# Optimization experiments

Hardware: AMD Instinct MI355X
Metric: run time of the kernel (lower is better)

The kernel has to match this reference:

```python
import jax, jax.numpy as jnp
import numpy as np

B, S, DIM, HEADS, DH = 1, 192, 512, 8, 64
LN_EPS = 1e-5


def setup_inputs() -> dict:
    key = jax.random.key(0)
    ks = jax.random.split(key, 5)
    rn = lambda k, shp: jax.random.normal(k, shp, dtype=jnp.float32) * 0.02
    return {
        "x": jax.random.normal(ks[0], (B, S, DIM), dtype=jnp.float32),
        "ln_w": jnp.ones((DIM,), jnp.float32),
        "ln_b": jnp.zeros((DIM,), jnp.float32),
        "W_abcde": rn(ks[1], (5 * HEADS * DH, DIM)),
        "b_abcde": jnp.zeros((5 * HEADS * DH,), jnp.float32),
        "W_K": rn(ks[2], (HEADS, DH, DH, DH)),
        "W_V": rn(ks[3], (HEADS, DH, DH, DH)),
        "W_out": rn(ks[4], (DIM, HEADS * DH)),
        "b_out": jnp.zeros((DIM,), jnp.float32),
    }


def reference(x, ln_w, ln_b, W_abcde, b_abcde, W_K, W_V, W_out, b_out):
    b, n, _ = x.shape
    # LayerNorm (biased variance, eps=1e-5, affine)
    mu = jnp.mean(x, axis=-1, keepdims=True)
    var = jnp.var(x, axis=-1, keepdims=True)
    xn = (x - mu) / jnp.sqrt(var + LN_EPS) * ln_w + ln_b
    # abcde projection, chunk into 5, split heads -> [b, n, h, d]
    proj = xn @ W_abcde.T + b_abcde
    a_, b_, c_, d_, e_ = [t.reshape(b, n, HEADS, DH) for t in jnp.split(proj, 5, axis=-1)]
    # cubic attention score chain (note: heads summed out in step2, reintroduced by a_)
    step1 = jnp.einsum('brnk,nijk->brij', c_, W_K)          # [b, r, d, d]
    step2 = jnp.einsum('brij,bqnj->briq', step1, b_)        # [b, r, d, q] (sum over heads of b_)
    attn = jnp.einsum('briq,bpni->bnpqr', step2, a_)        # [b, h, p, q, r]
    # "causal" mask: positions where p >= q set to 1e-6 (faithful to masked_fill_)
    t_idx = jnp.arange(n)[:, None, None]
    s_idx = jnp.arange(n)[None, :, None]
    mask = (t_idx >= s_idx)[None, None]                      # [1,1,p,q,1]
    attn = jnp.where(mask, jnp.float32(1e-6), attn)
    # 'b n p1 p2 p3 -> b n p3 (p1 p2)', scale by 1/dim_head, softmax over (p1 p2)
    attn = attn.transpose(0, 1, 4, 2, 3).reshape(b, HEADS, n, n * n) / DH
    attn = jax.nn.softmax(attn, axis=-1)
    # pairwise values: [b, p1, p2, h, d] -> 'b p s n h -> b n h (p s)'
    v = jnp.einsum('bpnh,bqng,nhgf->bpqnf', d_, e_, W_V)
    v = v.transpose(0, 3, 4, 1, 2).reshape(b, HEADS, DH, n * n)
    # weighted sum over pair axis, merge heads
    z = jnp.einsum('bnql,bnhl->bqnh', attn, v).reshape(b, n, HEADS * DH)
    return z @ W_out.T + b_out
```

## Files before the change

### kernel.cpp

```cpp
#include <hip/hip_runtime.h>
#include <hip/hip_bf16.h>
#include <cstdint>

#define SEQ 192

typedef float f32x4 __attribute__((ext_vector_type(4)));
typedef float f32x8 __attribute__((ext_vector_type(8)));
typedef __bf16 bf16;
typedef __bf16 bf16x8 __attribute__((ext_vector_type(8)));
typedef __bf16 bf16x4 __attribute__((ext_vector_type(4)));

#define MFMA_BF16(a, b, c) __builtin_amdgcn_mfma_f32_16x16x32_bf16(a, b, c, 0, 0, 0)

__device__ __forceinline__ bf16x8 cvt8(f32x8 v) {
  bf16x8 o;
#pragma unroll
  for (int i = 0; i < 8; i++) o[i] = (bf16)v[i];
  return o;
}

__global__ __launch_bounds__(256) void k1_prep(
    const float* __restrict__ x, const float* __restrict__ ln_w, const float* __restrict__ ln_b,
    const float* __restrict__ WV, bf16* __restrict__ xn_bf, bf16* __restrict__ WVt2) {
  int bid = blockIdx.x, tid = threadIdx.x;
  if (bid < 512) {
    int g = bid & 63, hh = bid >> 6;
    __shared__ float ld[64 * 65];
    int f = tid & 63, r4 = tid >> 6;
#pragma unroll
    for (int it = 0; it < 16; it++) {
      int hp = it * 4 + r4;
      ld[hp * 65 + f] = WV[(((size_t)(hh * 64 + hp) * 64 + g) * 64) + f];
    }
    __syncthreads();
    int hp2 = tid & 63;
#pragma unroll
    for (int it = 0; it < 16; it++) {
      int ff = it * 4 + r4;
      WVt2[(size_t)hh * 262144 + (size_t)(ff * 64 + g) * 64 + hp2] = (bf16)ld[hp2 * 65 + ff];
    }
    return;
  }
  bid -= 512;
  {
    int r = bid;
    const float* xr = x + (size_t)r * 512;
    float v0 = xr[tid], v1 = xr[tid + 256];
    float s = v0 + v1, s2 = v0 * v0 + v1 * v1;
#pragma unroll
    for (int off = 32; off > 0; off >>= 1) {
      s += __shfl_down(s, off);
      s2 += __shfl_down(s2, off);
    }
    __shared__ float redS[4], redS2[4];
    int wave = tid >> 6, lane = tid & 63;
    if (lane == 0) { redS[wave] = s; redS2[wave] = s2; }
    __syncthreads();
    float S = redS[0] + redS[1] + redS[2] + redS[3];
    float S2 = redS2[0] + redS2[1] + redS2[2] + redS2[3];
    float mean = S * (1.0f / 512.0f);
    float var = S2 * (1.0f / 512.0f) - mean * mean;
    float rstd = rsqrtf(var + 1e-5f);
    bf16* xnr = xn_bf + (size_t)r * 512;
    xnr[tid] = (bf16)((v0 - mean) * rstd * ln_w[tid] + ln_b[tid]);
    xnr[tid + 256] = (bf16)((v1 - mean) * rstd * ln_w[tid + 256] + ln_b[tid + 256]);
  }
}

__device__ __forceinline__ void gemm_rm(const bf16* __restrict__ A, const bf16* __restrict__ Bt,
                                        bf16* __restrict__ C1, int N, int K, int nb, int mb,
                                        int tid) {
  int n0 = nb * 64, m0 = mb * 64;
  int wave = tid >> 6, lane = tid & 63;
  int lq = lane >> 4, l16 = lane & 15;
  const bf16* Ap = A + (size_t)(m0 + wave * 16 + l16) * K;
  f32x4 acc[4];
#pragma unroll
  for (int nt = 0; nt < 4; nt++) acc[nt] = (f32x4){0.f, 0.f, 0.f, 0.f};
  for (int k0 = 0; k0 < K; k0 += 32) {
    bf16x8 af = *(const bf16x8*)(Ap + k0 + lq * 8);
#pragma unroll
    for (int nt = 0; nt < 4; nt++) {
      bf16x8 bv = *(const bf16x8*)(Bt + (size_t)(n0 + nt * 16 + l16) * K + k0 + lq * 8);
      acc[nt] = MFMA_BF16(af, bv, acc[nt]);
    }
  }
  int cm = m0 + wave * 16 + lq * 4;
#pragma unroll
  for (int nt = 0; nt < 4; nt++) {
    int n = n0 + nt * 16 + l16;
#pragma unroll
    for (int rg = 0; rg < 4; rg++) C1[(size_t)(cm + rg) * N + n] = (bf16)acc[nt][rg];
  }
}

__global__ __launch_bounds__(256) void k2_proj(
    const bf16* __restrict__ xn_bf, const float* __restrict__ Wab,
    const float* __restrict__ b_abcde, float* __restrict__ proj, bf16* __restrict__ a_bf,
    bf16* __restrict__ c_bf, bf16* __restrict__ d_bf) {
  int bid = blockIdx.x, tid = threadIdx.x;
  int nb = bid % 40, mb = bid / 40;
  int n0 = nb * 64, m0 = mb * 64;
  int wave = tid >> 6, lane = tid & 63;
  int lq = lane >> 4, l16 = lane & 15;
  const bf16* Ap = xn_bf + (size_t)(m0 + wave * 16 + l16) * 512;
  f32x4 acc[4];
#pragma unroll
  for (int nt = 0; nt < 4; nt++) acc[nt] = (f32x4){0.f, 0.f, 0.f, 0.f};
  for (int k0 = 0; k0 < 512; k0 += 32) {
    bf16x8 af = *(const bf16x8*)(Ap + k0 + lq * 8);
#pragma unroll
    for (int nt = 0; nt < 4; nt++) {
      f32x8 wv = *(const f32x8*)(Wab + (size_t)(n0 + nt * 16 + l16) * 512 + k0 + lq * 8);
      acc[nt] = MFMA_BF16(af, cvt8(wv), acc[nt]);
    }
  }
  int cm = m0 + wave * 16 + lq * 4;
#pragma unroll
  for (int nt = 0; nt < 4; nt++) {
    int n = n0 + nt * 16 + l16;
    int chunk = n >> 9, hcol = (n >> 6) & 7, i = n & 63;
#pragma unroll
    for (int rg = 0; rg < 4; rg++) {
      int m = cm + rg;
      float v = acc[nt][rg] + b_abcde[n];
      proj[(size_t)m * 2560 + n] = v;
      bf16 bv = (bf16)v;
      if (chunk == 0) a_bf[((size_t)hcol * SEQ + m) * 64 + i] = bv;
      else if (chunk == 2) c_bf[(size_t)m * 512 + (n - 1024)] = bv;
      else if (chunk == 3) d_bf[((size_t)hcol * SEQ + m) * 64 + i] = bv;
    }
  }
}

__global__ __launch_bounds__(256) void k3_mid(
    const bf16* __restrict__ c_bf, const float* __restrict__ WK, bf16* __restrict__ s1bf,
    const bf16* __restrict__ d_bf, const bf16* __restrict__ WVt2, bf16* __restrict__ tTt,
    const float* __restrict__ proj, bf16* __restrict__ eT_bf, float* __restrict__ ecum,
    bf16* __restrict__ bsum_bf) {
  __shared__ float el[64 * 65];
  int bid = blockIdx.x, tid = threadIdx.x;
  if (bid < 192) {
    int nb = bid % 64, mb = bid / 64;
    int n0 = nb * 64, m0 = mb * 64;
    int wave = tid >> 6, lane = tid & 63;
    int lq = lane >> 4, l16 = lane & 15;
    const bf16* Ap = c_bf + (size_t)(m0 + wave * 16 + l16) * 512;
    f32x4 acc[4];
#pragma unroll
    for (int nt = 0; nt < 4; nt++) acc[nt] = (f32x4){0.f, 0.f, 0.f, 0.f};
    size_t offn[4];
#pragma unroll
    for (int nt = 0; nt < 4; nt++) {
      int n = n0 + nt * 16 + l16;
      offn[nt] = (size_t)(n >> 6) * 4096 + (size_t)(n & 63) * 64;
    }
    for (int k0 = 0; k0 < 512; k0 += 32) {
      bf16x8 af = *(const bf16x8*)(Ap + k0 + lq * 8);
      size_t kb = (size_t)(k0 >> 6) * 262144 + (k0 & 32) + lq * 8;
#pragma unroll
      for (int nt = 0; nt < 4; nt++) {
        f32x8 wv = *(const f32x8*)(WK + kb + offn[nt]);
        acc[nt] = MFMA_BF16(af, cvt8(wv), acc[nt]);
      }
    }
    int cm = m0 + wave * 16 + lq * 4;
#pragma unroll
    for (int nt = 0; nt < 4; nt++) {
      int n = n0 + nt * 16 + l16;
#pragma unroll
      for (int rg = 0; rg < 4; rg++) s1bf[(size_t)(cm + rg) * 4096 + n] = (bf16)acc[nt][rg];
    }
    return;
  }
  bid -= 192;
  if (bid < 1536) {
    int h = bid / 192, rem = bid % 192;
    gemm_rm(d_bf + (size_t)h * 12288, WVt2 + (size_t)h * 262144,
            tTt + (size_t)h * 786432, 4096, 64, rem % 64, rem / 64, tid);
    return;
  }
  bid -= 1536;
  if (bid < 8) {
    int h = bid;
    float carry = 0.f;
    for (int ch = 0; ch < 3; ch++) {
      int pbase = ch * 64;
      if (ch) __syncthreads();
      for (int idx = tid; idx < 4096; idx += 256) {
        int pl = idx >> 6, g = idx & 63;
        el[pl * 65 + g] = proj[(size_t)(pbase + pl) * 2560 + 2048 + h * 64 + g];
      }
      __syncthreads();
      for (int idx = tid; idx < 4096; idx += 256) {
        int g = idx >> 6, ql = idx & 63;
        eT_bf[((size_t)h * 64 + g) * SEQ + pbase + ql] = (bf16)el[ql * 65 + g];
      }
      if (tid < 64) {
        float run = carry;
        for (int pl = 0; pl < 64; pl++) {
          run += el[pl * 65 + tid];
          ecum[(size_t)h * 12288 + (pbase + pl) * 64 + tid] = run;
        }
        carry = run;
      }
      __syncthreads();
    }
    return;
  }
  bid -= 8;
  {
    int j = tid & 63, qg = tid >> 6;
#pragma unroll
    for (int qi = 0; qi < 16; qi++) {
      int q = bid * 64 + qg * 16 + qi;
      float s = 0.f;
#pragma unroll
      for (int hh = 0; hh < 8; hh++) s += proj[(size_t)q * 2560 + 512 + hh * 64 + j];
      bsum_bf[q * 64 + j] = (bf16)s;
    }
  }
}

__global__ __launch_bounds__(256) void k4_step2(const bf16* __restrict__ s1bf,
                                                const bf16* __restrict__ bsum_bf,
                                                bf16* __restrict__ s2bf) {
  int bid = blockIdx.x, tid = threadIdx.x;
  int nb = bid % 3, mb = bid / 3;
  int n0 = nb * 64, m0 = mb * 64;
  int wave = tid >> 6, lane = tid & 63;
  int lq = lane >> 4, l16 = lane & 15;
  const bf16* Ap = s1bf + (size_t)(m0 + wave * 16 + l16) * 64;
  f32x4 acc[4];
#pragma unroll
  for (int nt = 0; nt < 4; nt++) acc[nt] = (f32x4){0.f, 0.f, 0.f, 0.f};
#pragma unroll
  for (int k0 = 0; k0 < 64; k0 += 32) {
    bf16x8 af = *(const bf16x8*)(Ap + k0 + lq * 8);
#pragma unroll
    for (int nt = 0; nt < 4; nt++) {
      bf16x8 bv = *(const bf16x8*)(bsum_bf + (size_t)(n0 + nt * 16 + l16) * 64 + k0 + lq * 8);
      acc[nt] = MFMA_BF16(af, bv, acc[nt]);
    }
  }
  int cm = m0 + wave * 16 + lq * 4;
#pragma unroll
  for (int nt = 0; nt < 4; nt++) {
    int n = n0 + nt * 16 + l16;
    int r = cm >> 6, i0 = cm & 63;
    bf16x4 pk = {(bf16)acc[nt][0], (bf16)acc[nt][1], (bf16)acc[nt][2], (bf16)acc[nt][3]};
    *(bf16x4*)(s2bf + (size_t)r * 12288 + (size_t)n * 64 + i0) = pk;
  }
}

__global__ __launch_bounds__(256, 3) void k5_attn(
    const bf16* __restrict__ a_bf, const bf16* __restrict__ s2bf,
    const bf16* __restrict__ eT_bf, const float* __restrict__ ecum,
    bf16* __restrict__ ew_bf, float* __restrict__ Lsum) {
  int r = blockIdx.x, h = blockIdx.y;
  int tid = threadIdx.x, wave = tid >> 6, lane = tid & 63;
  int lq = lane >> 4, l16 = lane & 15;
  __shared__ __align__(16) bf16 wch[4][3][16 * 40];
  __shared__ float redL[4];
  int pt[3] = {wave, wave + 4, 11 - wave};

  const bf16* ah = a_bf + (size_t)h * 12288;
  const bf16* s2r = s2bf + (size_t)r * 12288;
  const bf16* eh = eT_bf + (size_t)h * 12288;
  const float* ech = ecum + (size_t)h * 12288;

  bf16x8 afr[3][2];
#pragma unroll
  for (int mt = 0; mt < 3; mt++)
#pragma unroll
    for (int kc = 0; kc < 2; kc++)
      afr[mt][kc] = *(const bf16x8*)(ah + (pt[mt] * 16 + l16) * 64 + kc * 32 + lq * 8);

  f32x4 ewacc[3][4];
#pragma unroll
  for (int mt = 0; mt < 3; mt++)
#pragma unroll
    for (int nt = 0; nt < 4; nt++) ewacc[mt][nt] = (f32x4){0.f, 0.f, 0.f, 0.f};
  float lpart = 0.f;

  for (int cc = 0; cc < 6; cc++) {
    if (cc * 32 + 31 <= wave * 16) continue;
    bf16x8 efr[4];
#pragma unroll
    for (int nt = 0; nt < 4; nt++)
      efr[nt] = *(const bf16x8*)(eh + (nt * 16 + l16) * SEQ + cc * 32 + lq * 8);
    bf16x8 bq[2][2];
#pragma unroll
    for (int sub = 0; sub < 2; sub++) {
      int q = cc * 32 + sub * 16 + l16;
      bq[sub][0] = *(const bf16x8*)(s2r + q * 64 + lq * 8);
      bq[sub][1] = *(const bf16x8*)(s2r + q * 64 + 32 + lq * 8);
    }
    f32x4 sacc[3][2];
#pragma unroll
    for (int mt = 0; mt < 3; mt++) {
      if (cc * 32 + 31 <= pt[mt] * 16) continue;
#pragma unroll
      for (int sub = 0; sub < 2; sub++) {
        if (cc * 32 + sub * 16 + 15 <= pt[mt] * 16) continue;
        f32x4 sv = (f32x4){0.f, 0.f, 0.f, 0.f};
        sv = MFMA_BF16(afr[mt][0], bq[sub][0], sv);
        sacc[mt][sub] = MFMA_BF16(afr[mt][1], bq[sub][1], sv);
      }
    }
#pragma unroll
    for (int mt = 0; mt < 3; mt++) {
      if (cc * 32 + 31 <= pt[mt] * 16) continue;
      bf16* mybuf = &wch[wave][mt][0];
#pragma unroll
      for (int sub = 0; sub < 2; sub++) {
        if (cc * 32 + sub * 16 + 15 <= pt[mt] * 16) {
#pragma unroll
          for (int rg = 0; rg < 4; rg++) mybuf[(lq * 4 + rg) * 40 + sub * 16 + l16] = (bf16)0.f;
          continue;
        }
        int q = cc * 32 + sub * 16 + l16;
        int p0 = pt[mt] * 16 + lq * 4;
#pragma unroll
        for (int rg = 0; rg < 4; rg++) {
          float wv = (q > p0 + rg) ? __expf(sacc[mt][sub][rg] * 0.015625f) : 0.f;
          lpart += wv;
          mybuf[(lq * 4 + rg) * 40 + sub * 16 + l16] = (bf16)wv;
        }
      }
    }
#pragma unroll
    for (int mt = 0; mt < 3; mt++) {
      if (cc * 32 + 31 <= pt[mt] * 16) continue;
      bf16x8 wf = *(const bf16x8*)(&wch[wave][mt][l16 * 40 + lq * 8]);
#pragma unroll
      for (int nt = 0; nt < 4; nt++) ewacc[mt][nt] = MFMA_BF16(wf, efr[nt], ewacc[mt][nt]);
    }
  }

  bf16* ewout = ew_bf + ((size_t)h * SEQ + r) * 12288;
#pragma unroll
  for (int mt = 0; mt < 3; mt++)
#pragma unroll
    for (int nt = 0; nt < 4; nt++)
#pragma unroll
      for (int rg = 0; rg < 4; rg++) {
        int pp = pt[mt] * 16 + lq * 4 + rg;
        int g = nt * 16 + l16;
        ewout[pp * 64 + g] = (bf16)(ewacc[mt][nt][rg] + ech[pp * 64 + g]);
      }

#pragma unroll
  for (int off = 32; off > 0; off >>= 1) lpart += __shfl_down(lpart, off);
  if (lane == 0) redL[wave] = lpart;
  __syncthreads();
  if (tid == 0) Lsum[h * SEQ + r] = redL[0] + redL[1] + redL[2] + redL[3];
}

__global__ __launch_bounds__(256) void k5b_z(
    const bf16* __restrict__ ew_bf, const bf16* __restrict__ tTt, float* __restrict__ Zpart) {
  int h = blockIdx.x, mtb = blockIdx.y, ks = blockIdx.z;
  int tid = threadIdx.x, wave = tid >> 6, lane = tid & 63;
  int lq = lane >> 4, l16 = lane & 15;
  __shared__ float zred[4 * 16 * 66];
  const bf16* ewh = ew_bf + ((size_t)h * SEQ + mtb * 32) * 12288;
  const bf16* th = tTt + (size_t)h * 786432;
  f32x4 acc[2][4];
#pragma unroll
  for (int m2 = 0; m2 < 2; m2++)
#pragma unroll
    for (int nt = 0; nt < 4; nt++) acc[m2][nt] = (f32x4){0.f, 0.f, 0.f, 0.f};
#pragma unroll
  for (int jj = 0; jj < 6; jj++) {
    int kc = ks * 24 + wave * 6 + jj;
    int pp = kc >> 1, g0 = (kc & 1) * 32;
    bf16x8 af0 = *(const bf16x8*)(ewh + (size_t)l16 * 12288 + kc * 32 + lq * 8);
    bf16x8 af1 = *(const bf16x8*)(ewh + (size_t)(16 + l16) * 12288 + kc * 32 + lq * 8);
#pragma unroll
    for (int nt = 0; nt < 4; nt++) {
      bf16x8 tf = *(const bf16x8*)(th + (size_t)pp * 4096 + (nt * 16 + l16) * 64 + g0 + lq * 8);
      acc[0][nt] = MFMA_BF16(af0, tf, acc[0][nt]);
      acc[1][nt] = MFMA_BF16(af1, tf, acc[1][nt]);
    }
  }
#pragma unroll
  for (int m2 = 0; m2 < 2; m2++) {
    if (m2) __syncthreads();
#pragma unroll
    for (int nt = 0; nt < 4; nt++)
#pragma unroll
      for (int rg = 0; rg < 4; rg++)
        zred[(wave * 16 + lq * 4 + rg) * 66 + nt * 16 + l16] = acc[m2][nt][rg];
    __syncthreads();
#pragma unroll
    for (int o = 0; o < 4; o++) {
      int idx = o * 256 + tid;
      int rloc = idx >> 6, f = idx & 63;
      float s = zred[rloc * 66 + f] + zred[(16 + rloc) * 66 + f] + zred[(32 + rloc) * 66 + f] +
                zred[(48 + rloc) * 66 + f];
      Zpart[(size_t)ks * 98304 + (size_t)(mtb * 32 + m2 * 16 + rloc) * 512 + h * 64 + f] = s;
    }
  }
}

__global__ __launch_bounds__(256) void k6_out(
    const float* __restrict__ Zpart, const float* __restrict__ Lsum,
    const float* __restrict__ Wout, const float* __restrict__ b_out, float* __restrict__ out) {
  int u = blockIdx.x, tid = threadIdx.x;
  int mb = u >> 3, nb = u & 7;
  __shared__ __align__(16) bf16 zt[16 * 520];
  __shared__ float rd[4 * 16 * 68];
  for (int idx = tid; idx < 8192; idx += 256) {
    int m = idx >> 9, cc = idx & 511;
    float s = 0.f;
#pragma unroll
    for (int ks = 0; ks < 16; ks++)
      s += Zpart[(size_t)ks * 98304 + (size_t)(mb * 16 + m) * 512 + cc];
    float L = Lsum[(cc >> 6) * SEQ + mb * 16 + m] + 18528.0f;
    zt[m * 520 + cc] = (bf16)(s / L);
  }
  __syncthreads();
  int wave = tid >> 6, lane = tid & 63;
  int lq = lane >> 4, l16 = lane & 15;
  f32x4 acc[4];
#pragma unroll
  for (int nt = 0; nt < 4; nt++) acc[nt] = (f32x4){0.f, 0.f, 0.f, 0.f};
#pragma unroll
  for (int kc = 0; kc < 4; kc++) {
    int k0 = wave * 128 + kc * 32;
    bf16x8 af = *(const bf16x8*)(zt + l16 * 520 + k0 + lq * 8);
#pragma unroll
    for (int nt = 0; nt < 4; nt++) {
      f32x8 wv = *(const f32x8*)(Wout + (size_t)(nb * 64 + nt * 16 + l16) * 512 + k0 + lq * 8);
      acc[nt] = MFMA_BF16(af, cvt8(wv), acc[nt]);
    }
  }
#pragma unroll
  for (int nt = 0; nt < 4; nt++)
#pragma unroll
    for (int rg = 0; rg < 4; rg++)
      rd[(wave * 16 + lq * 4 + rg) * 68 + nt * 16 + l16] = acc[nt][rg];
  __syncthreads();
#pragma unroll
  for (int o = 0; o < 4; o++) {
    int idx = o * 256 + tid;
    int rloc = idx >> 6, f = idx & 63;
    float s = rd[rloc * 68 + f] + rd[(16 + rloc) * 68 + f] + rd[(32 + rloc) * 68 + f] +
              rd[(48 + rloc) * 68 + f];
    out[(size_t)(mb * 16 + rloc) * 512 + nb * 64 + f] = s + b_out[nb * 64 + f];
  }
}

static const size_t OFF_PROJ = 0;
static const size_t OFF_ECUM = 491520;
static const size_t OFF_XN = 589824;
static const size_t OFF_LSUM = 638976;
static const size_t OFF_ZPART = 640512;
static const size_t OFF_WVT = 2213376;
static const size_t OFF_A = 3261952;
static const size_t OFF_C = 3311104;
static const size_t OFF_D = 3360256;
static const size_t OFF_ET = 3409408;
static const size_t OFF_BSUM = 3458560;
static const size_t OFF_S1 = 3464704;
static const size_t OFF_TT = 5037568;
static const size_t OFF_EW = 8183296;
static const size_t OFF_S2 = 17620480;

extern "C" void kernel_launch(void* const* d_in, const int* in_sizes, int n_in,
                              void* d_out, int out_size, void* d_ws, size_t ws_size,
                              hipStream_t stream) {
  (void)in_sizes; (void)n_in; (void)out_size; (void)ws_size;
  const float* x = (const float*)d_in[0];
  const float* ln_w = (const float*)d_in[1];
  const float* ln_b = (const float*)d_in[2];
  const float* W_abcde = (const float*)d_in[3];
  const float* b_abcde = (const float*)d_in[4];
  const float* W_K = (const float*)d_in[5];
  const float* W_V = (const float*)d_in[6];
  const float* W_out = (const float*)d_in[7];
  const float* b_out = (const float*)d_in[8];
  float* out = (float*)d_out;
  float* ws = (float*)d_ws;

  float* proj = ws + OFF_PROJ;
  float* ecum = ws + OFF_ECUM;
  bf16* xn_bf = (bf16*)(ws + OFF_XN);
  float* Lsum = ws + OFF_LSUM;
  float* Zpart = ws + OFF_ZPART;
  bf16* WVt2 = (bf16*)(ws + OFF_WVT);
  bf16* a_bf = (bf16*)(ws + OFF_A);
  bf16* c_bf = (bf16*)(ws + OFF_C);
  bf16* d_bf = (bf16*)(ws + OFF_D);
  bf16* eT_bf = (bf16*)(ws + OFF_ET);
  bf16* bsum_bf = (bf16*)(ws + OFF_BSUM);
  bf16* s1bf = (bf16*)(ws + OFF_S1);
  bf16* tTt = (bf16*)(ws + OFF_TT);
  bf16* ew_bf = (bf16*)(ws + OFF_EW);
  bf16* s2bf = (bf16*)(ws + OFF_S2);

  k1_prep<<<704, 256, 0, stream>>>(x, ln_w, ln_b, W_V, xn_bf, WVt2);
  k2_proj<<<120, 256, 0, stream>>>(xn_bf, W_abcde, b_abcde, proj, a_bf, c_bf, d_bf);
  k3_mid<<<1739, 256, 0, stream>>>(c_bf, W_K, s1bf, d_bf, WVt2, tTt, proj, eT_bf, ecum,
                                   bsum_bf);
  k4_step2<<<576, 256, 0, stream>>>(s1bf, bsum_bf, s2bf);
  k5_attn<<<dim3(SEQ, 8), 256, 0, stream>>>(a_bf, s2bf, eT_bf, ecum, ew_bf, Lsum);
  k5b_z<<<dim3(8, 6, 16), 256, 0, stream>>>(ew_bf, tTt, Zpart);
  k6_out<<<96, 256, 0, stream>>>(Zpart, Lsum, W_out, b_out, out);
}
```

Measured before the change: 219.5 us.

## Factor ecum out of per-row ew and fold it into z via extra GEMM row

Instead of adding the cumulative e-sum (ecum) to every r-row of ew in k5_attn, the cumulative sum is written once per head as an extra row (row 192) of ew, and the z GEMM treats it as an additional M row. A new k5c_zf kernel adds that shared term to every output row and normalizes by L. k6_out then reads the precomputed bf16 z. k5b_z moves to 512-thread blocks with 8 waves and half as many k-splits. This removes the fp32 ecum reads in k5_attn and reduces the Zpart reduction. The cost is an extra kernel launch and a partially wasted 7th M tile, and the cumsum row is now rounded to bf16.

Result: no change. 219.8 us (+0.1%).

```diff
diff --git a/kernel.cpp b/kernel.cpp
--- a/kernel.cpp
+++ b/kernel.cpp
@@ -11,6 +11,8 @@
 typedef __bf16 bf16x4 __attribute__((ext_vector_type(4)));
 
 #define MFMA_BF16(a, b, c) __builtin_amdgcn_mfma_f32_16x16x32_bf16(a, b, c, 0, 0, 0)
+
+#define EWROWS 224
 
 __device__ __forceinline__ bf16x8 cvt8(f32x8 v) {
   bf16x8 o;
@@ -136,7 +138,7 @@
 __global__ __launch_bounds__(256) void k3_mid(
     const bf16* __restrict__ c_bf, const float* __restrict__ WK, bf16* __restrict__ s1bf,
     const bf16* __restrict__ d_bf, const bf16* __restrict__ WVt2, bf16* __restrict__ tTt,
-    const float* __restrict__ proj, bf16* __restrict__ eT_bf, float* __restrict__ ecum,
+    const float* __restrict__ proj, bf16* __restrict__ eT_bf, bf16* __restrict__ ew_bf,
     bf16* __restrict__ bsum_bf) {
   __shared__ float el[64 * 65];
   int bid = blockIdx.x, tid = threadIdx.x;
@@ -183,6 +185,7 @@
   bid -= 1536;
   if (bid < 8) {
     int h = bid;
+    bf16* vmrow = ew_bf + ((size_t)h * EWROWS + 192) * 12288;
     float carry = 0.f;
     for (int ch = 0; ch < 3; ch++) {
       int pbase = ch * 64;
@@ -200,7 +203,7 @@
         float run = carry;
         for (int pl = 0; pl < 64; pl++) {
           run += el[pl * 65 + tid];
-          ecum[(size_t)h * 12288 + (pbase + pl) * 64 + tid] = run;
+          vmrow[(pbase + pl) * 64 + tid] = (bf16)run;
         }
         carry = run;
       }
@@ -255,8 +258,7 @@
 
 __global__ __launch_bounds__(256, 3) void k5_attn(
     const bf16* __restrict__ a_bf, const bf16* __restrict__ s2bf,
-    const bf16* __restrict__ eT_bf, const float* __restrict__ ecum,
-    bf16* __restrict__ ew_bf, float* __restrict__ Lsum) {
+    const bf16* __restrict__ eT_bf, bf16* __restrict__ ew_bf, float* __restrict__ Lsum) {
   int r = blockIdx.x, h = blockIdx.y;
   int tid = threadIdx.x, wave = tid >> 6, lane = tid & 63;
   int lq = lane >> 4, l16 = lane & 15;
@@ -267,7 +269,6 @@
   const bf16* ah = a_bf + (size_t)h * 12288;
   const bf16* s2r = s2bf + (size_t)r * 12288;
   const bf16* eh = eT_bf + (size_t)h * 12288;
-  const float* ech = ecum + (size_t)h * 12288;
 
   bf16x8 afr[3][2];
 #pragma unroll
@@ -338,7 +339,7 @@
     }
   }
 
-  bf16* ewout = ew_bf + ((size_t)h * SEQ + r) * 12288;
+  bf16* ewout = ew_bf + ((size_t)h * EWROWS + r) * 12288;
 #pragma unroll
   for (int mt = 0; mt < 3; mt++)
 #pragma unroll
@@ -347,7 +348,7 @@
       for (int rg = 0; rg < 4; rg++) {
         int pp = pt[mt] * 16 + lq * 4 + rg;
         int g = nt * 16 + l16;
-        ewout[pp * 64 + g] = (bf16)(ewacc[mt][nt][rg] + ech[pp * 64 + g]);
+        ewout[pp * 64 + g] = (bf16)ewacc[mt][nt][rg];
       }
 
 #pragma unroll
@@ -357,22 +358,21 @@
   if (tid == 0) Lsum[h * SEQ + r] = redL[0] + redL[1] + redL[2] + redL[3];
 }
 
-__global__ __launch_bounds__(256) void k5b_z(
+__global__ __launch_bounds__(512) void k5b_z(
     const bf16* __restrict__ ew_bf, const bf16* __restrict__ tTt, float* __restrict__ Zpart) {
-  int h = blockIdx.x, mtb = blockIdx.y, ks = blockIdx.z;
+  int h = blockIdx.x, mt = blockIdx.y, ks = blockIdx.z;
   int tid = threadIdx.x, wave = tid >> 6, lane = tid & 63;
   int lq = lane >> 4, l16 = lane & 15;
-  __shared__ float zred[4 * 16 * 66];
-  const bf16* ewh = ew_bf + ((size_t)h * SEQ + mtb * 32) * 12288;
+  __shared__ float zred[8][16][66];
+  const bf16* ewh = ew_bf + ((size_t)h * EWROWS + mt * 32) * 12288;
   const bf16* th = tTt + (size_t)h * 786432;
   f32x4 acc[2][4];
 #pragma unroll
   for (int m2 = 0; m2 < 2; m2++)
 #pragma unroll
     for (int nt = 0; nt < 4; nt++) acc[m2][nt] = (f32x4){0.f, 0.f, 0.f, 0.f};
-#pragma unroll
   for (int jj = 0; jj < 6; jj++) {
-    int kc = ks * 24 + wave * 6 + jj;
+    int kc = ks * 48 + wave * 6 + jj;
     int pp = kc >> 1, g0 = (kc & 1) * 32;
     bf16x8 af0 = *(const bf16x8*)(ewh + (size_t)l16 * 12288 + kc * 32 + lq * 8);
     bf16x8 af1 = *(const bf16x8*)(ewh + (size_t)(16 + l16) * 12288 + kc * 32 + lq * 8);
@@ -385,87 +385,95 @@
   }
 #pragma unroll
   for (int m2 = 0; m2 < 2; m2++) {
+    if (mt == 6 && m2 == 1) break;
     if (m2) __syncthreads();
 #pragma unroll
     for (int nt = 0; nt < 4; nt++)
 #pragma unroll
-      for (int rg = 0; rg < 4; rg++)
-        zred[(wave * 16 + lq * 4 + rg) * 66 + nt * 16 + l16] = acc[m2][nt][rg];
+      for (int rg = 0; rg < 4; rg++) zred[wave][lq * 4 + rg][nt * 16 + l16] = acc[m2][nt][rg];
     __syncthreads();
 #pragma unroll
-    for (int o = 0; o < 4; o++) {
-      int idx = o * 256 + tid;
+    for (int o = 0; o < 2; o++) {
+      int idx = o * 512 + tid;
       int rloc = idx >> 6, f = idx & 63;
-      float s = zred[rloc * 66 + f] + zred[(16 + rloc) * 66 + f] + zred[(32 + rloc) * 66 + f] +
-                zred[(48 + rloc) * 66 + f];
-      Zpart[(size_t)ks * 98304 + (size_t)(mtb * 32 + m2 * 16 + rloc) * 512 + h * 64 + f] = s;
-    }
+      float s = 0.f;
+#pragma unroll
+      for (int wv = 0; wv < 8; wv++) s += zred[wv][rloc][f];
+      Zpart[(size_t)ks * 106496 + (size_t)(mt * 32 + m2 * 16 + rloc) * 512 + h * 64 + f] = s;
+    }
+  }
+}
+
+__global__ __launch_bounds__(256) void k5c_zf(const float* __restrict__ Zpart,
+                                              const float* __restrict__ Lsum,
+                                              bf16* __restrict__ z_bf) {
+  int m = blockIdx.x, tid = threadIdx.x;
+#pragma unroll
+  for (int o = 0; o < 2; o++) {
+    int c = o * 256 + tid;
+    int h = c >> 6;
+    float s = 0.f, vm = 0.f;
+#pragma unroll
+    for (int ks = 0; ks < 8; ks++) {
+      s += Zpart[(size_t)ks * 106496 + (size_t)m * 512 + c];
+      vm += Zpart[(size_t)ks * 106496 + (size_t)192 * 512 + c];
+    }
+    float L = Lsum[h * SEQ + m] + 18528.0f;
+    z_bf[(size_t)m * 512 + c] = (bf16)((s + vm) / L);
   }
 }
 
 __global__ __launch_bounds__(256) void k6_out(
-    const float* __restrict__ Zpart, const float* __restrict__ Lsum,
-    const float* __restrict__ Wout, const float* __restrict__ b_out, float* __restrict__ out) {
-  int u = blockIdx.x, tid = threadIdx.x;
-  int mb = u >> 3, nb = u & 7;
-  __shared__ __align__(16) bf16 zt[16 * 520];
-  __shared__ float rd[4 * 16 * 68];
-  for (int idx = tid; idx < 8192; idx += 256) {
-    int m = idx >> 9, cc = idx & 511;
-    float s = 0.f;
-#pragma unroll
-    for (int ks = 0; ks < 16; ks++)
-      s += Zpart[(size_t)ks * 98304 + (size_t)(mb * 16 + m) * 512 + cc];
-    float L = Lsum[(cc >> 6) * SEQ + mb * 16 + m] + 18528.0f;
-    zt[m * 520 + cc] = (bf16)(s / L);
-  }
-  __syncthreads();
+    const bf16* __restrict__ z_bf, const float* __restrict__ Wout,
+    const float* __restrict__ b_out, float* __restrict__ out) {
+  int bid = blockIdx.x, tid = threadIdx.x;
+  int nb = bid & 7, mb = bid >> 3;
   int wave = tid >> 6, lane = tid & 63;
   int lq = lane >> 4, l16 = lane & 15;
+  int m = mb * 16 + l16;
   f32x4 acc[4];
 #pragma unroll
   for (int nt = 0; nt < 4; nt++) acc[nt] = (f32x4){0.f, 0.f, 0.f, 0.f};
 #pragma unroll
   for (int kc = 0; kc < 4; kc++) {
     int k0 = wave * 128 + kc * 32;
-    bf16x8 af = *(const bf16x8*)(zt + l16 * 520 + k0 + lq * 8);
+    bf16x8 af = *(const bf16x8*)(z_bf + (size_t)m * 512 + k0 + lq * 8);
 #pragma unroll
     for (int nt = 0; nt < 4; nt++) {
       f32x8 wv = *(const f32x8*)(Wout + (size_t)(nb * 64 + nt * 16 + l16) * 512 + k0 + lq * 8);
       acc[nt] = MFMA_BF16(af, cvt8(wv), acc[nt]);
     }
   }
+  __shared__ float red[4][16][68];
 #pragma unroll
   for (int nt = 0; nt < 4; nt++)
 #pragma unroll
-    for (int rg = 0; rg < 4; rg++)
-      rd[(wave * 16 + lq * 4 + rg) * 68 + nt * 16 + l16] = acc[nt][rg];
+    for (int rg = 0; rg < 4; rg++) red[wave][lq * 4 + rg][nt * 16 + l16] = acc[nt][rg];
   __syncthreads();
 #pragma unroll
   for (int o = 0; o < 4; o++) {
     int idx = o * 256 + tid;
     int rloc = idx >> 6, f = idx & 63;
-    float s = rd[rloc * 68 + f] + rd[(16 + rloc) * 68 + f] + rd[(32 + rloc) * 68 + f] +
-              rd[(48 + rloc) * 68 + f];
+    float s = red[0][rloc][f] + red[1][rloc][f] + red[2][rloc][f] + red[3][rloc][f];
     out[(size_t)(mb * 16 + rloc) * 512 + nb * 64 + f] = s + b_out[nb * 64 + f];
   }
 }
 
 static const size_t OFF_PROJ = 0;
-static const size_t OFF_ECUM = 491520;
-static const size_t OFF_XN = 589824;
-static const size_t OFF_LSUM = 638976;
-static const size_t OFF_ZPART = 640512;
-static const size_t OFF_WVT = 2213376;
-static const size_t OFF_A = 3261952;
-static const size_t OFF_C = 3311104;
-static const size_t OFF_D = 3360256;
-static const size_t OFF_ET = 3409408;
-static const size_t OFF_BSUM = 3458560;
-static const size_t OFF_S1 = 3464704;
-static const size_t OFF_TT = 5037568;
-static const size_t OFF_EW = 8183296;
-static const size_t OFF_S2 = 17620480;
+static const size_t OFF_XN = 491520;
+static const size_t OFF_LSUM = 540672;
+static const size_t OFF_ZPART = 542208;
+static const size_t OFF_WVT = 1394176;
+static const size_t OFF_A = 2442752;
+static const size_t OFF_C = 2491904;
+static const size_t OFF_D = 2541056;
+static const size_t OFF_ET = 2590208;
+static const size_t OFF_BSUM = 2639360;
+static const size_t OFF_S1 = 2645504;
+static const size_t OFF_S2 = 3038720;
+static const size_t OFF_TT = 4218368;
+static const size_t OFF_Z = 7364096;
+static const size_t OFF_EW = 7413248;
 
 extern "C" void kernel_launch(void* const* d_in, const int* in_sizes, int n_in,
                               void* d_out, int out_size, void* d_ws, size_t ws_size,
@@ -484,7 +492,6 @@
   float* ws = (float*)d_ws;
 
   float* proj = ws + OFF_PROJ;
-  float* ecum = ws + OFF_ECUM;
   bf16* xn_bf = (bf16*)(ws + OFF_XN);
   float* Lsum = ws + OFF_LSUM;
   float* Zpart = ws + OFF_ZPART;
@@ -495,16 +502,18 @@
   bf16* eT_bf = (bf16*)(ws + OFF_ET);
   bf16* bsum_bf = (bf16*)(ws + OFF_BSUM);
   bf16* s1bf = (bf16*)(ws + OFF_S1);
+  bf16* s2bf = (bf16*)(ws + OFF_S2);
   bf16* tTt = (bf16*)(ws + OFF_TT);
+  bf16* z_bf = (bf16*)(ws + OFF_Z);
   bf16* ew_bf = (bf16*)(ws + OFF_EW);
-  bf16* s2bf = (bf16*)(ws + OFF_S2);
 
   k1_prep<<<704, 256, 0, stream>>>(x, ln_w, ln_b, W_V, xn_bf, WVt2);
   k2_proj<<<120, 256, 0, stream>>>(xn_bf, W_abcde, b_abcde, proj, a_bf, c_bf, d_bf);
-  k3_mid<<<1739, 256, 0, stream>>>(c_bf, W_K, s1bf, d_bf, WVt2, tTt, proj, eT_bf, ecum,
+  k3_mid<<<1739, 256, 0, stream>>>(c_bf, W_K, s1bf, d_bf, WVt2, tTt, proj, eT_bf, ew_bf,
                                    bsum_bf);
   k4_step2<<<576, 256, 0, stream>>>(s1bf, bsum_bf, s2bf);
-  k5_attn<<<dim3(SEQ, 8), 256, 0, stream>>>(a_bf, s2bf, eT_bf, ecum, ew_bf, Lsum);
-  k5b_z<<<dim3(8, 6, 16), 256, 0, stream>>>(ew_bf, tTt, Zpart);
-  k6_out<<<96, 256, 0, stream>>>(Zpart, Lsum, W_out, b_out, out);
-}
+  k5_attn<<<dim3(SEQ, 8), 256, 0, stream>>>(a_bf, s2bf, eT_bf, ew_bf, Lsum);
+  k5b_z<<<dim3(8, 7, 8), 512, 0, stream>>>(ew_bf, tTt, Zpart);
+  k5c_zf<<<SEQ, 256, 0, stream>>>(Zpart, Lsum, z_bf);
+  k6_out<<<96, 256, 0, stream>>>(z_bf, W_out, b_out, out);
+}
```
